# Optimization experiments

Measured on AMD Instinct MI355X. Metric: run time of the kernel, lower is better.

## Reference

```python
import jax, jax.numpy as jnp
import numpy as np

NUM_HEADS = 16


def setup_inputs() -> dict:
    key = jax.random.key(0)
    k1, k2, k3, k4, k5 = jax.random.split(key, 5)
    B, N, E = 16, 8, 2048
    H = NUM_HEADS
    D = E // H
    KV = 4096
    return {
        "x": jax.random.normal(k1, (B, N, E), dtype=jnp.float32),
        "past_k": jax.random.normal(k2, (B, H, KV, D), dtype=jnp.float32),
        "past_v": jax.random.normal(k3, (B, H, KV, D), dtype=jnp.float32),
        "W_qkv": jax.random.normal(k4, (3 * E, E), dtype=jnp.float32) * (E ** -0.5),
        "W_out": jax.random.normal(k5, (E, E), dtype=jnp.float32) * (E ** -0.5),
    }


def reference(x, past_k, past_v, W_qkv, W_out):
    B, N, E = x.shape
    H = NUM_HEADS
    D = E // H
    # fused QKV projection: [B, N, 3E]
    qkv = jnp.einsum("bne,fe->bnf", x, W_qkv)
    q, k_new, v_new = jnp.split(qkv, 3, axis=-1)
    # '... n (h d) -> ... h n d'
    to_heads = lambda t: t.reshape(B, N, H, D).swapaxes(1, 2)
    q, k_new, v_new = to_heads(q), to_heads(k_new), to_heads(v_new)
    # KV cache append along seq dim
    k = jnp.concatenate([past_k, k_new], axis=-2)  # [B, H, KV+N, D]
    v = jnp.concatenate([past_v, v_new], axis=-2)
    # SDPA (eval mode -> is_causal=False)
    scale = D ** -0.5
    scores = jnp.einsum("bhqd,bhkd->bhqk", q, k) * scale
    attn = jax.nn.softmax(scores, axis=-1)
    out = jnp.einsum("bhqk,bhkd->bhqd", attn, v)  # [B, H, N, D]
    # '... h n d -> ... n (h d)'
    out = out.swapaxes(1, 2).reshape(B, N, E)
    out = jnp.einsum("bne,fe->bnf", out, W_out)
    return (out, k, v)
```

## Files before the change

### kernel.cpp

```cpp
#include <hip/hip_runtime.h>
#include <cstddef>
#include <cstdint>

#define B_ 16
#define H_ 16
#define NQ 8
#define D_ 128
#define E_ 2048
#define F3 6144
#define KVP 4096
#define KVT 4104
#define SCALE 0.08838834764831843f
#define NCHUNK 16
#define CHUNK 256
#define PARTSZ 1040
#define QKV_N 786432
#define ATTN_N 262144

#define WAVE_LDS_FENCE() asm volatile("s_waitcnt lgkmcnt(0)" ::: "memory")

template <int BM, int BN, int SPLITK>
__global__ __launch_bounds__(256) void gemm_xwt(const float* __restrict__ X,
                                                const float* __restrict__ W,
                                                float* __restrict__ C,
                                                int K, int Fdim) {
  constexpr int BK = 32;
  constexpr int RM = BM / 16;
  constexpr int RN = BN / 16;
  __shared__ float xs[BK][BM + 4];
  __shared__ float wss[BK][BN + 4];
  const int t = threadIdx.x;
  const int tm = t >> 4, tn = t & 15;
  const int m0 = blockIdx.y * BM, f0 = blockIdx.x * BN;
  const int kbeg = (SPLITK > 1) ? blockIdx.z * (K / SPLITK) : 0;
  const int kend = (SPLITK > 1) ? kbeg + K / SPLITK : K;
  if (SPLITK > 1) C += (size_t)blockIdx.z * 128 * Fdim;
  float acc[RM][RN];
#pragma unroll
  for (int i = 0; i < RM; ++i)
#pragma unroll
    for (int j = 0; j < RN; ++j) acc[i][j] = 0.f;

  for (int kk = kbeg; kk < kend; kk += BK) {
#pragma unroll
    for (int i = 0; i < (BM * BK) / 1024; ++i) {
      int j = t + i * 256;
      int r = j >> 3;
      int c = (j & 7) << 2;
      float4 v = *reinterpret_cast<const float4*>(&X[(size_t)(m0 + r) * K + kk + c]);
      xs[c + 0][r] = v.x; xs[c + 1][r] = v.y; xs[c + 2][r] = v.z; xs[c + 3][r] = v.w;
    }
#pragma unroll
    for (int i = 0; i < (BN * BK) / 1024; ++i) {
      int j = t + i * 256;
      int r = j >> 3;
      int c = (j & 7) << 2;
      float4 v = *reinterpret_cast<const float4*>(&W[(size_t)(f0 + r) * K + kk + c]);
      wss[c + 0][r] = v.x; wss[c + 1][r] = v.y; wss[c + 2][r] = v.z; wss[c + 3][r] = v.w;
    }
    __syncthreads();
#pragma unroll
    for (int k = 0; k < BK; ++k) {
      float xv[RM], wv[RN];
      if constexpr (RM == 4) {
        *reinterpret_cast<float4*>(xv) = *reinterpret_cast<const float4*>(&xs[k][tm * 4]);
      } else {
        *reinterpret_cast<float2*>(xv) = *reinterpret_cast<const float2*>(&xs[k][tm * 2]);
      }
      if constexpr (RN == 4) {
        *reinterpret_cast<float4*>(wv) = *reinterpret_cast<const float4*>(&wss[k][tn * 4]);
      } else {
        *reinterpret_cast<float2*>(wv) = *reinterpret_cast<const float2*>(&wss[k][tn * 2]);
      }
#pragma unroll
      for (int i = 0; i < RM; ++i)
#pragma unroll
        for (int j = 0; j < RN; ++j) acc[i][j] += xv[i] * wv[j];
    }
    __syncthreads();
  }
#pragma unroll
  for (int i = 0; i < RM; ++i) {
    float* cp = &C[(size_t)(m0 + tm * RM + i) * Fdim + f0 + tn * RN];
    if constexpr (RN == 4) {
      *reinterpret_cast<float4*>(cp) = make_float4(acc[i][0], acc[i][1], acc[i][2], acc[i][3]);
    } else {
      *reinterpret_cast<float2*>(cp) = make_float2(acc[i][0], acc[i][1]);
    }
  }
}

__global__ __launch_bounds__(256) void add4(const float* __restrict__ a,
                                            float* __restrict__ o, int n) {
  int i = blockIdx.x * 256 + threadIdx.x;
  const float4* a4 = reinterpret_cast<const float4*>(a);
  int n4 = n >> 2;
  float4 v0 = a4[i], v1 = a4[i + n4], v2 = a4[i + 2 * n4], v3 = a4[i + 3 * n4];
  reinterpret_cast<float4*>(o)[i] =
      make_float4(v0.x + v1.x + v2.x + v3.x, v0.y + v1.y + v2.y + v3.y,
                  v0.z + v1.z + v2.z + v3.z, v0.w + v1.w + v2.w + v3.w);
}

__global__ __launch_bounds__(256) void attn_partial(
    const float* __restrict__ past_k, const float* __restrict__ past_v,
    const float* __restrict__ qkv,
    float* __restrict__ out_k, float* __restrict__ out_v,
    float* __restrict__ part) {
  const int t = threadIdx.x;
  const int c = blockIdx.x, h = blockIdx.y, b = blockIdx.z;
  const int bh = b * H_ + h;
  const int l = t & 63, w = t >> 6;
  const int g = l & 31, half = l >> 5;

  __shared__ float red[4096];
  __shared__ float pw_s[4][72];
  __shared__ float mw_lds[32], lw_lds[32];
  float* p_w = pw_s[w];
  float* f_w = pw_s[w] + 64;

  float4 qreg[NQ];
#pragma unroll
  for (int qi = 0; qi < NQ; ++qi) {
    const size_t qoff = (size_t)(b * NQ + qi) * F3 + h * D_ + g * 4;
    float4 q0 = *reinterpret_cast<const float4*>(&qkv[qoff]);
    q0.x *= SCALE; q0.y *= SCALE; q0.z *= SCALE; q0.w *= SCALE;
    qreg[qi] = q0;
  }

  const int wbase = w * 64;
  const float* gk = past_k + ((size_t)bh * KVP + (size_t)c * CHUNK) * D_;
  const float* gv = past_v + ((size_t)bh * KVP + (size_t)c * CHUNK) * D_;
  float* ok = out_k + ((size_t)bh * KVT + (size_t)c * CHUNK) * D_;
  float* ov = out_v + ((size_t)bh * KVT + (size_t)c * CHUNK) * D_;

  float4 acc[NQ];
#pragma unroll
  for (int qi = 0; qi < NQ; ++qi) acc[qi] = make_float4(0.f, 0.f, 0.f, 0.f);
  float m_run = -1e30f, l_run = 0.f;

  const int b0 = g & 1, b1 = (g >> 1) & 1, b2 = (g >> 2) & 1;
  const int qsel = 4 * b0 + 2 * b1 + b2;
  const int cp = g >> 3;

  auto body = [&](float4 (&kf)[4], float4 (&kn)[4], int it, bool pf) {
    float4 vf[4];
#pragma unroll
    for (int j = 0; j < 4; ++j) {
      const size_t ga = (size_t)(wbase + it * 8 + half + 2 * j) * D_ + g * 4;
      vf[j] = *reinterpret_cast<const float4*>(&gv[ga]);
    }
    float s4[4];
#pragma unroll
    for (int j = 0; j < 4; ++j) {
      float sp[NQ];
#pragma unroll
      for (int qi = 0; qi < NQ; ++qi)
        sp[qi] = kf[j].x * qreg[qi].x + kf[j].y * qreg[qi].y +
                 kf[j].z * qreg[qi].z + kf[j].w * qreg[qi].w;
      float v1[4];
#pragma unroll
      for (int jj = 0; jj < 4; ++jj) {
        float x = b0 ? sp[jj] : sp[jj + 4];
        v1[jj] = (b0 ? sp[jj + 4] : sp[jj]) + __shfl_xor(x, 1);
      }
      float v2[2];
#pragma unroll
      for (int jj = 0; jj < 2; ++jj) {
        float x = b1 ? v1[jj] : v1[jj + 2];
        v2[jj] = (b1 ? v1[jj + 2] : v1[jj]) + __shfl_xor(x, 2);
      }
      float v3;
      {
        float x = b2 ? v2[0] : v2[1];
        v3 = (b2 ? v2[1] : v2[0]) + __shfl_xor(x, 4);
      }
      v3 += __shfl_xor(v3, 8);
      v3 += __shfl_xor(v3, 16);
      s4[j] = v3;
    }
    {
      float mt = fmaxf(fmaxf(s4[0], s4[1]), fmaxf(s4[2], s4[3]));
      mt = fmaxf(mt, __shfl_xor(mt, 32));
      float mn = fmaxf(m_run, mt);
      float f = __expf(m_run - mn);
      s4[0] = __expf(s4[0] - mn);
      s4[1] = __expf(s4[1] - mn);
      s4[2] = __expf(s4[2] - mn);
      s4[3] = __expf(s4[3] - mn);
      float ps = (s4[0] + s4[1]) + (s4[2] + s4[3]);
      ps += __shfl_xor(ps, 32);
      l_run = l_run * f + ps;
      m_run = mn;
      p_w[(half + 2 * cp) * 8 + qsel] = s4[cp];
      if (l < 8) f_w[qsel] = f;
    }
    WAVE_LDS_FENCE();

    if (pf) {
#pragma unroll
      for (int j = 0; j < 4; ++j) {
        const size_t ga = (size_t)(wbase + (it + 1) * 8 + half + 2 * j) * D_ + g * 4;
        kn[j] = *reinterpret_cast<const float4*>(&gk[ga]);
      }
    }

    {
      float4 f0 = *reinterpret_cast<const float4*>(&f_w[0]);
      float4 f1 = *reinterpret_cast<const float4*>(&f_w[4]);
      acc[0].x *= f0.x; acc[0].y *= f0.x; acc[0].z *= f0.x; acc[0].w *= f0.x;
      acc[1].x *= f0.y; acc[1].y *= f0.y; acc[1].z *= f0.y; acc[1].w *= f0.y;
      acc[2].x *= f0.z; acc[2].y *= f0.z; acc[2].z *= f0.z; acc[2].w *= f0.z;
      acc[3].x *= f0.w; acc[3].y *= f0.w; acc[3].z *= f0.w; acc[3].w *= f0.w;
      acc[4].x *= f1.x; acc[4].y *= f1.x; acc[4].z *= f1.x; acc[4].w *= f1.x;
      acc[5].x *= f1.y; acc[5].y *= f1.y; acc[5].z *= f1.y; acc[5].w *= f1.y;
      acc[6].x *= f1.z; acc[6].y *= f1.z; acc[6].z *= f1.z; acc[6].w *= f1.z;
      acc[7].x *= f1.w; acc[7].y *= f1.w; acc[7].z *= f1.w; acc[7].w *= f1.w;
#pragma unroll
      for (int j = 0; j < 4; ++j) {
        const int r = half + 2 * j;
        float4 pa = *reinterpret_cast<const float4*>(&p_w[r * 8]);
        float4 pc4 = *reinterpret_cast<const float4*>(&p_w[r * 8 + 4]);
        acc[0].x += pa.x * vf[j].x; acc[0].y += pa.x * vf[j].y; acc[0].z += pa.x * vf[j].z; acc[0].w += pa.x * vf[j].w;
        acc[1].x += pa.y * vf[j].x; acc[1].y += pa.y * vf[j].y; acc[1].z += pa.y * vf[j].z; acc[1].w += pa.y * vf[j].w;
        acc[2].x += pa.z * vf[j].x; acc[2].y += pa.z * vf[j].y; acc[2].z += pa.z * vf[j].z; acc[2].w += pa.z * vf[j].w;
        acc[3].x += pa.w * vf[j].x; acc[3].y += pa.w * vf[j].y; acc[3].z += pa.w * vf[j].z; acc[3].w += pa.w * vf[j].w;
        acc[4].x += pc4.x * vf[j].x; acc[4].y += pc4.x * vf[j].y; acc[4].z += pc4.x * vf[j].z; acc[4].w += pc4.x * vf[j].w;
        acc[5].x += pc4.y * vf[j].x; acc[5].y += pc4.y * vf[j].y; acc[5].z += pc4.y * vf[j].z; acc[5].w += pc4.y * vf[j].w;
        acc[6].x += pc4.z * vf[j].x; acc[6].y += pc4.z * vf[j].y; acc[6].z += pc4.z * vf[j].z; acc[6].w += pc4.z * vf[j].w;
        acc[7].x += pc4.w * vf[j].x; acc[7].y += pc4.w * vf[j].y; acc[7].z += pc4.w * vf[j].z; acc[7].w += pc4.w * vf[j].w;
      }
    }

#pragma unroll
    for (int j = 0; j < 4; ++j) {
      const size_t ga = (size_t)(wbase + it * 8 + half + 2 * j) * D_ + g * 4;
      *reinterpret_cast<float4*>(&ok[ga]) = kf[j];
      *reinterpret_cast<float4*>(&ov[ga]) = vf[j];
    }
  };

  float4 kA[4], kB[4];
#pragma unroll
  for (int j = 0; j < 4; ++j)
    kA[j] = *reinterpret_cast<const float4*>(&gk[(size_t)(wbase + half + 2 * j) * D_ + g * 4]);

  for (int it = 0; it < 8; it += 2) {
    body(kA, kB, it, true);
    body(kB, kA, it + 1, it + 2 < 8);
  }

#pragma unroll
  for (int qi = 0; qi < NQ; ++qi) {
    acc[qi].x += __shfl_xor(acc[qi].x, 32);
    acc[qi].y += __shfl_xor(acc[qi].y, 32);
    acc[qi].z += __shfl_xor(acc[qi].z, 32);
    acc[qi].w += __shfl_xor(acc[qi].w, 32);
  }

  if (l < 8) { mw_lds[w * 8 + qsel] = m_run; lw_lds[w * 8 + qsel] = l_run; }
  if (half == 0) {
#pragma unroll
    for (int qi = 0; qi < NQ; ++qi)
      *reinterpret_cast<float4*>(&red[w * 1024 + qi * 128 + g * 4]) = acc[qi];
  }
  __syncthreads();

  {
    const int col4 = t & 31, qi = (t >> 5) & 7;
    float M = mw_lds[qi];
    M = fmaxf(M, mw_lds[8 + qi]);
    M = fmaxf(M, mw_lds[16 + qi]);
    M = fmaxf(M, mw_lds[24 + qi]);
    float den = 0.f;
    float4 num = make_float4(0.f, 0.f, 0.f, 0.f);
#pragma unroll
    for (int ww = 0; ww < 4; ++ww) {
      float wt = __expf(mw_lds[ww * 8 + qi] - M);
      den += wt * lw_lds[ww * 8 + qi];
      float4 a = *reinterpret_cast<const float4*>(&red[ww * 1024 + qi * 128 + col4 * 4]);
      num.x += wt * a.x; num.y += wt * a.y; num.z += wt * a.z; num.w += wt * a.w;
    }
    float* pb = part + ((size_t)bh * NCHUNK + c) * PARTSZ;
    *reinterpret_cast<float4*>(&pb[16 + qi * 128 + col4 * 4]) = num;
    if (col4 == 0) { pb[qi] = M; pb[8 + qi] = den; }
  }
}

__global__ __launch_bounds__(256) void attn_combine(
    const float* __restrict__ qkv,
    const float* __restrict__ part, float* __restrict__ out_k,
    float* __restrict__ out_v, float* __restrict__ attn) {
  const int t = threadIdx.x;
  const int h = blockIdx.x, b = blockIdx.y;
  const int bh = b * H_ + h;
  __shared__ float q_lds[NQ * 132];
  __shared__ float kn_lds[NQ * 132];
  __shared__ float vn_lds[NQ * 132];
  __shared__ float p9[NQ * 12];
  __shared__ float m9_lds[NQ], s9_lds[NQ];
  {
    int n = t >> 5, g = t & 31;
    const size_t soff = (size_t)(b * NQ + n) * F3 + h * D_ + g * 4;
    float4 qv = *reinterpret_cast<const float4*>(&qkv[soff]);
    float4 kv = *reinterpret_cast<const float4*>(&qkv[soff + E_]);
    float4 vv = *reinterpret_cast<const float4*>(&qkv[soff + 2 * E_]);
    *reinterpret_cast<float4*>(&q_lds[n * 132 + g * 4]) = qv;
    *reinterpret_cast<float4*>(&kn_lds[n * 132 + g * 4]) = kv;
    *reinterpret_cast<float4*>(&vn_lds[n * 132 + g * 4]) = vv;
    *reinterpret_cast<float4*>(&out_k[((size_t)bh * KVT + KVP + n) * D_ + g * 4]) = kv;
    *reinterpret_cast<float4*>(&out_v[((size_t)bh * KVT + KVP + n) * D_ + g * 4]) = vv;
  }
  __syncthreads();
  if (t < 64) {
    int nq = t >> 3, nk = t & 7;
    float s = 0.f;
#pragma unroll
    for (int g = 0; g < 32; ++g) {
      float4 qv = *reinterpret_cast<const float4*>(&q_lds[nq * 132 + g * 4]);
      float4 kv = *reinterpret_cast<const float4*>(&kn_lds[nk * 132 + g * 4]);
      s += qv.x * kv.x + qv.y * kv.y + qv.z * kv.z + qv.w * kv.w;
    }
    s *= SCALE;
    float mx = s;
#pragma unroll
    for (int o = 4; o > 0; o >>= 1) mx = fmaxf(mx, __shfl_xor(mx, o));
    float p = __expf(s - mx);
    float sm = p;
#pragma unroll
    for (int o = 4; o > 0; o >>= 1) sm += __shfl_xor(sm, o);
    p9[nk * 12 + nq] = p;
    if (nk == 0) { m9_lds[nq] = mx; s9_lds[nq] = sm; }
  }
  __syncthreads();
  const int qg = t >> 7, dcol = t & 127;
  const float* pb = part + (size_t)bh * NCHUNK * PARTSZ;
#pragma unroll
  for (int jq = 0; jq < 4; ++jq) {
    int qi = qg * 4 + jq;
    float M = m9_lds[qi];
#pragma unroll
    for (int c = 0; c < NCHUNK; ++c) M = fmaxf(M, pb[(size_t)c * PARTSZ + qi]);
    float num = 0.f, den = 0.f;
#pragma unroll
    for (int c = 0; c < NCHUNK; ++c) {
      const float* pc = pb + (size_t)c * PARTSZ;
      float wgt = __expf(pc[qi] - M);
      den += wgt * pc[8 + qi];
      num += wgt * pc[16 + (size_t)qi * D_ + dcol];
    }
    float acc9 = 0.f;
#pragma unroll
    for (int r = 0; r < NQ; ++r) acc9 += p9[r * 12 + qi] * vn_lds[r * 132 + dcol];
    float w9 = __expf(m9_lds[qi] - M);
    num += w9 * acc9;
    den += w9 * s9_lds[qi];
    attn[((size_t)(b * NQ + qi)) * E_ + h * D_ + dcol] = num / den;
  }
}

extern "C" void kernel_launch(void* const* d_in, const int* in_sizes, int n_in,
                              void* d_out, int out_size, void* d_ws, size_t ws_size,
                              hipStream_t stream) {
  const float* x      = (const float*)d_in[0];
  const float* past_k = (const float*)d_in[1];
  const float* past_v = (const float*)d_in[2];
  const float* W_qkv  = (const float*)d_in[3];
  const float* W_out  = (const float*)d_in[4];

  float* out   = (float*)d_out;
  float* out_k = out + (size_t)B_ * NQ * E_;
  float* out_v = out_k + (size_t)B_ * H_ * KVT * D_;

  const size_t PART_N = (size_t)B_ * H_ * NCHUNK * PARTSZ;
  const size_t need4  = (5 * (size_t)QKV_N + PART_N + 5 * (size_t)ATTN_N) * sizeof(float);

  float* ws = (float*)d_ws;
  const bool s4 = ws_size >= need4;

  float* pq   = ws;
  float* sq   = pq + 4 * (size_t)QKV_N;
  float* part = sq + QKV_N;
  float* attn = part + PART_N;
  float* po   = attn + ATTN_N;

  if (s4) {
    gemm_xwt<64, 64, 4><<<dim3(F3 / 64, 2, 4), 256, 0, stream>>>(x, W_qkv, pq, E_, F3);
    add4<<<dim3(QKV_N / 1024), 256, 0, stream>>>(pq, sq, QKV_N);
  } else {
    sq = ws; part = sq + QKV_N; attn = part + PART_N; po = attn + ATTN_N;
    gemm_xwt<64, 64, 1><<<dim3(F3 / 64, 2), 256, 0, stream>>>(x, W_qkv, sq, E_, F3);
  }
  attn_partial<<<dim3(NCHUNK, H_, B_), 256, 0, stream>>>(past_k, past_v, sq,
                                                         out_k, out_v, part);
  attn_combine<<<dim3(H_, B_), 256, 0, stream>>>(sq, part, out_k, out_v, attn);
  if (s4) {
    gemm_xwt<64, 64, 4><<<dim3(E_ / 64, 2, 4), 256, 0, stream>>>(attn, W_out, po, E_, E_);
    add4<<<dim3(ATTN_N / 1024), 256, 0, stream>>>(po, out, ATTN_N);
  } else {
    gemm_xwt<64, 64, 1><<<dim3(E_ / 64, 2), 256, 0, stream>>>(attn, W_out, out, E_, E_);
  }
}
```

Measured before the change: 513.4 us.

## Split PV accumulators across wave halves to cut registers and raise occupancy

```diff
diff --git a/kernel.cpp b/kernel.cpp
--- a/kernel.cpp
+++ b/kernel.cpp
@@ -101,7 +101,7 @@
                   v0.z + v1.z + v2.z + v3.z, v0.w + v1.w + v2.w + v3.w);
 }
 
-__global__ __launch_bounds__(256) void attn_partial(
+__global__ __launch_bounds__(256, 4) void attn_partial(
     const float* __restrict__ past_k, const float* __restrict__ past_v,
     const float* __restrict__ qkv,
     float* __restrict__ out_k, float* __restrict__ out_v,
@@ -133,9 +133,9 @@
   float* ok = out_k + ((size_t)bh * KVT + (size_t)c * CHUNK) * D_;
   float* ov = out_v + ((size_t)bh * KVT + (size_t)c * CHUNK) * D_;
 
-  float4 acc[NQ];
-#pragma unroll
-  for (int qi = 0; qi < NQ; ++qi) acc[qi] = make_float4(0.f, 0.f, 0.f, 0.f);
+  float4 acc[4];
+#pragma unroll
+  for (int jq = 0; jq < 4; ++jq) acc[jq] = make_float4(0.f, 0.f, 0.f, 0.f);
   float m_run = -1e30f, l_run = 0.f;
 
   const int b0 = g & 1, b1 = (g >> 1) & 1, b2 = (g >> 2) & 1;
@@ -205,29 +205,38 @@
     }
 
     {
-      float4 f0 = *reinterpret_cast<const float4*>(&f_w[0]);
-      float4 f1 = *reinterpret_cast<const float4*>(&f_w[4]);
-      acc[0].x *= f0.x; acc[0].y *= f0.x; acc[0].z *= f0.x; acc[0].w *= f0.x;
-      acc[1].x *= f0.y; acc[1].y *= f0.y; acc[1].z *= f0.y; acc[1].w *= f0.y;
-      acc[2].x *= f0.z; acc[2].y *= f0.z; acc[2].z *= f0.z; acc[2].w *= f0.z;
-      acc[3].x *= f0.w; acc[3].y *= f0.w; acc[3].z *= f0.w; acc[3].w *= f0.w;
-      acc[4].x *= f1.x; acc[4].y *= f1.x; acc[4].z *= f1.x; acc[4].w *= f1.x;
-      acc[5].x *= f1.y; acc[5].y *= f1.y; acc[5].z *= f1.y; acc[5].w *= f1.y;
-      acc[6].x *= f1.z; acc[6].y *= f1.z; acc[6].z *= f1.z; acc[6].w *= f1.z;
-      acc[7].x *= f1.w; acc[7].y *= f1.w; acc[7].z *= f1.w; acc[7].w *= f1.w;
+      float4 fq = *reinterpret_cast<const float4*>(&f_w[half * 4]);
+      acc[0].x *= fq.x; acc[0].y *= fq.x; acc[0].z *= fq.x; acc[0].w *= fq.x;
+      acc[1].x *= fq.y; acc[1].y *= fq.y; acc[1].z *= fq.y; acc[1].w *= fq.y;
+      acc[2].x *= fq.z; acc[2].y *= fq.z; acc[2].z *= fq.z; acc[2].w *= fq.z;
+      acc[3].x *= fq.w; acc[3].y *= fq.w; acc[3].z *= fq.w; acc[3].w *= fq.w;
 #pragma unroll
       for (int j = 0; j < 4; ++j) {
-        const int r = half + 2 * j;
-        float4 pa = *reinterpret_cast<const float4*>(&p_w[r * 8]);
-        float4 pc4 = *reinterpret_cast<const float4*>(&p_w[r * 8 + 4]);
-        acc[0].x += pa.x * vf[j].x; acc[0].y += pa.x * vf[j].y; acc[0].z += pa.x * vf[j].z; acc[0].w += pa.x * vf[j].w;
-        acc[1].x += pa.y * vf[j].x; acc[1].y += pa.y * vf[j].y; acc[1].z += pa.y * vf[j].z; acc[1].w += pa.y * vf[j].w;
-        acc[2].x += pa.z * vf[j].x; acc[2].y += pa.z * vf[j].y; acc[2].z += pa.z * vf[j].z; acc[2].w += pa.z * vf[j].w;
-        acc[3].x += pa.w * vf[j].x; acc[3].y += pa.w * vf[j].y; acc[3].z += pa.w * vf[j].z; acc[3].w += pa.w * vf[j].w;
-        acc[4].x += pc4.x * vf[j].x; acc[4].y += pc4.x * vf[j].y; acc[4].z += pc4.x * vf[j].z; acc[4].w += pc4.x * vf[j].w;
-        acc[5].x += pc4.y * vf[j].x; acc[5].y += pc4.y * vf[j].y; acc[5].z += pc4.y * vf[j].z; acc[5].w += pc4.y * vf[j].w;
-        acc[6].x += pc4.z * vf[j].x; acc[6].y += pc4.z * vf[j].y; acc[6].z += pc4.z * vf[j].z; acc[6].w += pc4.z * vf[j].w;
-        acc[7].x += pc4.w * vf[j].x; acc[7].y += pc4.w * vf[j].y; acc[7].z += pc4.w * vf[j].z; acc[7].w += pc4.w * vf[j].w;
+        const int ro = half + 2 * j;
+        const int rt = (half ^ 1) + 2 * j;
+        float4 po = *reinterpret_cast<const float4*>(&p_w[ro * 8 + half * 4]);
+        float4 pt = *reinterpret_cast<const float4*>(&p_w[rt * 8 + half * 4]);
+        float4 vt;
+        vt.x = __shfl_xor(vf[j].x, 32);
+        vt.y = __shfl_xor(vf[j].y, 32);
+        vt.z = __shfl_xor(vf[j].z, 32);
+        vt.w = __shfl_xor(vf[j].w, 32);
+        acc[0].x += po.x * vf[j].x + pt.x * vt.x;
+        acc[0].y += po.x * vf[j].y + pt.x * vt.y;
+        acc[0].z += po.x * vf[j].z + pt.x * vt.z;
+        acc[0].w += po.x * vf[j].w + pt.x * vt.w;
+        acc[1].x += po.y * vf[j].x + pt.y * vt.x;
+        acc[1].y += po.y * vf[j].y + pt.y * vt.y;
+        acc[1].z += po.y * vf[j].z + pt.y * vt.z;
+        acc[1].w += po.y * vf[j].w + pt.y * vt.w;
+        acc[2].x += po.z * vf[j].x + pt.z * vt.x;
+        acc[2].y += po.z * vf[j].y + pt.z * vt.y;
+        acc[2].z += po.z * vf[j].z + pt.z * vt.z;
+        acc[2].w += po.z * vf[j].w + pt.z * vt.w;
+        acc[3].x += po.w * vf[j].x + pt.w * vt.x;
+        acc[3].y += po.w * vf[j].y + pt.w * vt.y;
+        acc[3].z += po.w * vf[j].z + pt.w * vt.z;
+        acc[3].w += po.w * vf[j].w + pt.w * vt.w;
       }
     }
 
@@ -249,20 +258,10 @@
     body(kB, kA, it + 1, it + 2 < 8);
   }
 
-#pragma unroll
-  for (int qi = 0; qi < NQ; ++qi) {
-    acc[qi].x += __shfl_xor(acc[qi].x, 32);
-    acc[qi].y += __shfl_xor(acc[qi].y, 32);
-    acc[qi].z += __shfl_xor(acc[qi].z, 32);
-    acc[qi].w += __shfl_xor(acc[qi].w, 32);
-  }
-
   if (l < 8) { mw_lds[w * 8 + qsel] = m_run; lw_lds[w * 8 + qsel] = l_run; }
-  if (half == 0) {
-#pragma unroll
-    for (int qi = 0; qi < NQ; ++qi)
-      *reinterpret_cast<float4*>(&red[w * 1024 + qi * 128 + g * 4]) = acc[qi];
-  }
+#pragma unroll
+  for (int jq = 0; jq < 4; ++jq)
+    *reinterpret_cast<float4*>(&red[w * 1024 + (half * 4 + jq) * 128 + g * 4]) = acc[jq];
   __syncthreads();
 
   {
```

Result: slower. 1.056 ms (+105.7%).
